# Optimization experiments

Hardware: AMD Instinct MI355X
Metric: run time of the kernel (lower is better)

Reference implementation:

```python
import jax, jax.numpy as jnp
import numpy as np

TEMPERATURE = 0.5
EPS = 1e-12  # matches torch F.normalize default eps


def _l2_normalize(x):
    norm = jnp.sqrt(jnp.sum(x * x, axis=1, keepdims=True))
    return x / jnp.maximum(norm, EPS)


def setup_inputs() -> dict:
    key = jax.random.key(0)
    k1, k2 = jax.random.split(key)
    proj_1 = jax.random.normal(k1, (4096, 128), dtype=jnp.float32)
    proj_2 = jax.random.normal(k2, (4096, 128), dtype=jnp.float32)
    return {"proj_1": proj_1, "proj_2": proj_2}


def reference(proj_1, proj_2):
    batch_size = proj_1.shape[0]
    z_i = _l2_normalize(proj_1)
    z_j = _l2_normalize(proj_2)
    reps = jnp.concatenate([z_i, z_j], axis=0)  # [2B, D], rows unit-norm
    # cosine similarity of unit-norm rows == dot product -> single matmul
    sim = reps @ reps.T  # [2B, 2B]
    # positives: diag offset +B and -B
    pos_ij = jnp.diagonal(sim, offset=batch_size)   # [B]
    pos_ji = jnp.diagonal(sim, offset=-batch_size)  # [B]
    positives = jnp.concatenate([pos_ij, pos_ji], axis=0)  # [2B]
    nominator = jnp.exp(positives / TEMPERATURE)
    n = 2 * batch_size
    mask = 1.0 - jnp.eye(n, dtype=sim.dtype)
    denominator = jnp.sum(mask * jnp.exp(sim / TEMPERATURE), axis=1)  # [2B]
    all_losses = -jnp.log(nominator / denominator)
    return jnp.sum(all_losses) / n
```

## Files before the change

kernel.cpp:

```cpp
#include <hip/hip_runtime.h>
#include <stdint.h>


#define TEMP 0.5f
#define EXP2_SCALE 2.885390081777927f

typedef __bf16 bf16_t;
typedef bf16_t bf16x8 __attribute__((ext_vector_type(8)));
typedef float floatx4 __attribute__((ext_vector_type(4)));

typedef __attribute__((address_space(3))) uint32_t lds_u32;
typedef const __attribute__((address_space(1))) uint32_t glb_u32;

__device__ __forceinline__ unsigned short f32_to_bf16(float f) {
    union { float f; uint32_t u; } v; v.f = f;
    uint32_t u = v.u;
    uint32_t r = (u + 0x7FFFu + ((u >> 16) & 1u)) >> 16;
    return (unsigned short)r;
}

__device__ __forceinline__ bf16x8 as_bf16x8(uint4 v) {
    union { uint4 u; bf16x8 b; } c; c.u = v; return c.b;
}

__global__ __launch_bounds__(256) void norm_pos_kernel(
        const float* __restrict__ p1, const float* __restrict__ p2,
        unsigned short* __restrict__ reps, float* __restrict__ pos,
        float* __restrict__ rowsum, int B) {
    if (threadIdx.x < 16) {
        int z = blockIdx.x * 16 + threadIdx.x;
        if (z < 2 * B) rowsum[z] = 0.f;
    }

    const int wave = threadIdx.x >> 6;
    const int lane = threadIdx.x & 63;
    const int half = lane >> 5;
    const int h    = lane & 31;
    const int i = blockIdx.x * 8 + wave * 2 + half;
    if (i >= B) return;

    float4 a = ((const float4*)(p1 + (size_t)i * 128))[h];
    float4 b = ((const float4*)(p2 + (size_t)i * 128))[h];
    float ss1 = a.x * a.x + a.y * a.y + a.z * a.z + a.w * a.w;
    float ss2 = b.x * b.x + b.y * b.y + b.z * b.z + b.w * b.w;
    float d   = a.x * b.x + a.y * b.y + a.z * b.z + a.w * b.w;
    #pragma unroll
    for (int off = 16; off > 0; off >>= 1) {
        ss1 += __shfl_xor(ss1, off);
        ss2 += __shfl_xor(ss2, off);
        d   += __shfl_xor(d,   off);
    }
    float rn1 = rsqrtf(fmaxf(ss1, 1e-24f));
    float rn2 = rsqrtf(fmaxf(ss2, 1e-24f));

    ((ushort4*)reps)[(size_t)i * 32 + h] = make_ushort4(
        f32_to_bf16(a.x * rn1), f32_to_bf16(a.y * rn1),
        f32_to_bf16(a.z * rn1), f32_to_bf16(a.w * rn1));
    ((ushort4*)reps)[(size_t)(B + i) * 32 + h] = make_ushort4(
        f32_to_bf16(b.x * rn2), f32_to_bf16(b.y * rn2),
        f32_to_bf16(b.z * rn2), f32_to_bf16(b.w * rn2));

    if (h == 0) pos[i] = d * rn1 * rn2;
}

__global__ __launch_bounds__(256) void simexp_kernel(
        const unsigned short* __restrict__ reps,
        float* __restrict__ rowsum, int nt) {
    const int tid  = threadIdx.x;
    const int wave = tid >> 6;
    const int lane = tid & 63;
    const int quad = lane >> 4;
    const int l16  = lane & 15;

    int rem = (int)blockIdx.x;
    int by = 0;
    while (rem >= nt - by) { rem -= nt - by; ++by; }
    const int bx = by + rem;
    const bool diag = (bx == by);

    const int rowWave = by * 128 + wave * 32;
    const int colBase = bx * 128;

    const uint4* g = (const uint4*)reps;

    __shared__ __align__(16) unsigned short bbuf[8][2048];
    __shared__ float lds_cs[4][128];

    lds_cs[wave][lane]      = 0.f;
    lds_cs[wave][lane + 64] = 0.f;

    const int s_ks  = tid >> 6;
    const int s_fl  = tid & 63;
    const int s_fq  = s_fl >> 4;
    const int s_f16 = s_fl & 15;
    #pragma unroll
    for (int ct = 0; ct < 8; ++ct) {
        const unsigned short* src = reps
            + (size_t)(colBase + ct * 16 + s_f16) * 128 + s_ks * 32 + s_fq * 8;
        __builtin_amdgcn_global_load_lds(
            (glb_u32*)src, (lds_u32*)&bbuf[ct][tid * 8], 16, 0, 0);
    }

    bf16x8 a[2][4];
    #pragma unroll
    for (int t = 0; t < 2; ++t)
        #pragma unroll
        for (int ks = 0; ks < 4; ++ks)
            a[t][ks] = as_bf16x8(g[(size_t)(rowWave + t * 16 + l16) * 16 + ks * 4 + quad]);

    float rs[2][4];
    #pragma unroll
    for (int t = 0; t < 2; ++t)
        #pragma unroll
        for (int r = 0; r < 4; ++r) rs[t][r] = 0.f;

    __syncthreads();

    #pragma unroll 2
    for (int ct = 0; ct < 8; ++ct) {
        bf16x8 b[4];
        #pragma unroll
        for (int ks = 0; ks < 4; ++ks)
            b[ks] = *(const bf16x8*)&bbuf[ct][ks * 512 + lane * 8];

        floatx4 acc[2];
        #pragma unroll
        for (int t = 0; t < 2; ++t) acc[t] = (floatx4){0.f, 0.f, 0.f, 0.f};
        #pragma unroll
        for (int ks = 0; ks < 4; ++ks)
            #pragma unroll
            for (int t = 0; t < 2; ++t)
                acc[t] = __builtin_amdgcn_mfma_f32_16x16x32_bf16(a[t][ks], b[ks], acc[t], 0, 0, 0);

        const int c = colBase + ct * 16 + l16;
        if (!diag) {
            float cs = 0.f;
            #pragma unroll
            for (int t = 0; t < 2; ++t)
                #pragma unroll
                for (int r = 0; r < 4; ++r) {
                    float e = exp2f(acc[t][r] * EXP2_SCALE);
                    rs[t][r] += e;
                    cs += e;
                }
            cs += __shfl_xor(cs, 16);
            cs += __shfl_xor(cs, 32);
            if (lane < 16) lds_cs[wave][ct * 16 + lane] += cs;
        } else {
            #pragma unroll
            for (int t = 0; t < 2; ++t) {
                const int rb = rowWave + t * 16 + quad * 4;
                #pragma unroll
                for (int r = 0; r < 4; ++r) {
                    float e = (rb + r == c) ? 0.f : exp2f(acc[t][r] * EXP2_SCALE);
                    rs[t][r] += e;
                }
            }
        }
    }

    #pragma unroll
    for (int off = 1; off < 16; off <<= 1)
        #pragma unroll
        for (int t = 0; t < 2; ++t)
            #pragma unroll
            for (int r = 0; r < 4; ++r)
                rs[t][r] += __shfl_xor(rs[t][r], off);

    if (l16 == 0) {
        #pragma unroll
        for (int t = 0; t < 2; ++t)
            #pragma unroll
            for (int r = 0; r < 4; ++r)
                atomicAdd(&rowsum[rowWave + t * 16 + quad * 4 + r], rs[t][r]);
    }

    if (!diag) {
        __syncthreads();
        if (tid < 128)
            atomicAdd(&rowsum[colBase + tid],
                      lds_cs[0][tid] + lds_cs[1][tid] + lds_cs[2][tid] + lds_cs[3][tid]);
    }
}

__global__ __launch_bounds__(1024) void finalize_kernel(
        const float* __restrict__ rowsum, const float* __restrict__ pos,
        float* __restrict__ out, int N2, int B) {
    float v = 0.f;
    const float4* r4 = (const float4*)rowsum;
    const int n4 = N2 >> 2;
    for (int k = threadIdx.x; k < n4; k += 1024) {
        float4 x = r4[k];
        v += logf(x.x) + logf(x.y) + logf(x.z) + logf(x.w);
    }
    float p = 0.f;
    const float4* p4 = (const float4*)pos;
    const int b4 = B >> 2;
    for (int i = threadIdx.x; i < b4; i += 1024) {
        float4 x = p4[i];
        p += x.x + x.y + x.z + x.w;
    }
    float local = v * (1.0f / (float)N2) - p * (1.0f / ((float)B * TEMP));

    #pragma unroll
    for (int off = 32; off > 0; off >>= 1) local += __shfl_xor(local, off);

    __shared__ float wsum[16];
    int wave = threadIdx.x >> 6, lane = threadIdx.x & 63;
    if (lane == 0) wsum[wave] = local;
    __syncthreads();
    if (threadIdx.x == 0) {
        float s = 0.f;
        for (int i = 0; i < 16; ++i) s += wsum[i];
        out[0] = s;
    }
}

extern "C" void kernel_launch(void* const* d_in, const int* in_sizes, int n_in,
                              void* d_out, int out_size, void* d_ws, size_t ws_size,
                              hipStream_t stream) {
    const float* p1 = (const float*)d_in[0];
    const float* p2 = (const float*)d_in[1];
    float* out = (float*)d_out;

    const int B  = in_sizes[0] / 128;
    const int N2 = 2 * B;

    unsigned short* reps = (unsigned short*)d_ws;
    float* rowsum = (float*)((char*)d_ws + (size_t)N2 * 256);
    float* pos    = rowsum + N2;

    norm_pos_kernel<<<dim3((B + 7) / 8), dim3(256), 0, stream>>>(p1, p2, reps, pos, rowsum, B);

    const int nt = N2 / 128;
    const int nb = nt * (nt + 1) / 2;
    simexp_kernel<<<dim3(nb), dim3(256), 0, stream>>>(reps, rowsum, nt);

    finalize_kernel<<<dim3(1), dim3(1024), 0, stream>>>(rowsum, pos, out, N2, B);
}
```

Before: 91.51 us.

## Fuse normalize, sim-exp and finalize into one cooperative persistent kernel

The three kernels are merged into one persistent kernel launched cooperatively. Grid-wide syncs separate the normalize, similarity-exp and log-reduce phases, and blocks loop over the triangular tile list. Column sums are now kept in registers and atomically added per lane instead of being staged in LDS. Raw v_exp/v_log intrinsics are used, and the final reduction is spread across blocks with an atomicAdd to the output. The aim is to remove launch gaps and the single-block finalize, at the cost of grid-sync overhead, more global atomics, and a three-launch fallback path.

Measured after the change: 205.1 us. 2.24x slower.

```diff
diff --git a/kernel.cpp b/kernel.cpp
--- a/kernel.cpp
+++ b/kernel.cpp
@@ -1,5 +1,8 @@
 #include <hip/hip_runtime.h>
+#include <hip/hip_cooperative_groups.h>
 #include <stdint.h>
+
+namespace cg = cooperative_groups;
 
 
 #define TEMP 0.5f
@@ -23,196 +26,189 @@
     union { uint4 u; bf16x8 b; } c; c.u = v; return c.b;
 }
 
-__global__ __launch_bounds__(256) void norm_pos_kernel(
+__device__ __forceinline__ float exp2_raw(float x) {
+#if __has_builtin(__builtin_amdgcn_exp2f)
+    return __builtin_amdgcn_exp2f(x);
+#else
+    float r; asm("v_exp_f32 %0, %1" : "=v"(r) : "v"(x)); return r;
+#endif
+}
+__device__ __forceinline__ float log2_raw(float x) {
+#if __has_builtin(__builtin_amdgcn_logf)
+    return __builtin_amdgcn_logf(x);
+#else
+    float r; asm("v_log_f32 %0, %1" : "=v"(r) : "v"(x)); return r;
+#endif
+}
+
+__global__ __launch_bounds__(256, 4) void fused_kernel(
         const float* __restrict__ p1, const float* __restrict__ p2,
-        unsigned short* __restrict__ reps, float* __restrict__ pos,
-        float* __restrict__ rowsum, int B) {
-    if (threadIdx.x < 16) {
-        int z = blockIdx.x * 16 + threadIdx.x;
-        if (z < 2 * B) rowsum[z] = 0.f;
-    }
-
-    const int wave = threadIdx.x >> 6;
-    const int lane = threadIdx.x & 63;
-    const int half = lane >> 5;
-    const int h    = lane & 31;
-    const int i = blockIdx.x * 8 + wave * 2 + half;
-    if (i >= B) return;
-
-    float4 a = ((const float4*)(p1 + (size_t)i * 128))[h];
-    float4 b = ((const float4*)(p2 + (size_t)i * 128))[h];
-    float ss1 = a.x * a.x + a.y * a.y + a.z * a.z + a.w * a.w;
-    float ss2 = b.x * b.x + b.y * b.y + b.z * b.z + b.w * b.w;
-    float d   = a.x * b.x + a.y * b.y + a.z * b.z + a.w * b.w;
-    #pragma unroll
-    for (int off = 16; off > 0; off >>= 1) {
-        ss1 += __shfl_xor(ss1, off);
-        ss2 += __shfl_xor(ss2, off);
-        d   += __shfl_xor(d,   off);
-    }
-    float rn1 = rsqrtf(fmaxf(ss1, 1e-24f));
-    float rn2 = rsqrtf(fmaxf(ss2, 1e-24f));
-
-    ((ushort4*)reps)[(size_t)i * 32 + h] = make_ushort4(
-        f32_to_bf16(a.x * rn1), f32_to_bf16(a.y * rn1),
-        f32_to_bf16(a.z * rn1), f32_to_bf16(a.w * rn1));
-    ((ushort4*)reps)[(size_t)(B + i) * 32 + h] = make_ushort4(
-        f32_to_bf16(b.x * rn2), f32_to_bf16(b.y * rn2),
-        f32_to_bf16(b.z * rn2), f32_to_bf16(b.w * rn2));
-
-    if (h == 0) pos[i] = d * rn1 * rn2;
-}
-
-__global__ __launch_bounds__(256) void simexp_kernel(
-        const unsigned short* __restrict__ reps,
-        float* __restrict__ rowsum, int nt) {
+        float* __restrict__ out, unsigned short* __restrict__ reps,
+        float* __restrict__ rowsum, float* __restrict__ pos,
+        int B, int nt, int nb, int phase) {
     const int tid  = threadIdx.x;
     const int wave = tid >> 6;
     const int lane = tid & 63;
     const int quad = lane >> 4;
     const int l16  = lane & 15;
-
-    int rem = (int)blockIdx.x;
-    int by = 0;
-    while (rem >= nt - by) { rem -= nt - by; ++by; }
-    const int bx = by + rem;
-    const bool diag = (bx == by);
-
-    const int rowWave = by * 128 + wave * 32;
-    const int colBase = bx * 128;
-
-    const uint4* g = (const uint4*)reps;
+    const int G    = gridDim.x;
+    const int N2   = 2 * B;
 
     __shared__ __align__(16) unsigned short bbuf[8][2048];
-    __shared__ float lds_cs[4][128];
-
-    lds_cs[wave][lane]      = 0.f;
-    lds_cs[wave][lane + 64] = 0.f;
-
-    const int s_ks  = tid >> 6;
-    const int s_fl  = tid & 63;
-    const int s_fq  = s_fl >> 4;
-    const int s_f16 = s_fl & 15;
-    #pragma unroll
-    for (int ct = 0; ct < 8; ++ct) {
-        const unsigned short* src = reps
-            + (size_t)(colBase + ct * 16 + s_f16) * 128 + s_ks * 32 + s_fq * 8;
-        __builtin_amdgcn_global_load_lds(
-            (glb_u32*)src, (lds_u32*)&bbuf[ct][tid * 8], 16, 0, 0);
-    }
-
-    bf16x8 a[2][4];
-    #pragma unroll
-    for (int t = 0; t < 2; ++t)
+    __shared__ float wsum[4];
+
+    if (phase <= 1) {
+        const int slot = tid >> 5;
+        const int h    = tid & 31;
+        for (int i = blockIdx.x * 8 + slot; i < B; i += G * 8) {
+            float4 a = ((const float4*)(p1 + (size_t)i * 128))[h];
+            float4 b = ((const float4*)(p2 + (size_t)i * 128))[h];
+            float ss1 = a.x*a.x + a.y*a.y + a.z*a.z + a.w*a.w;
+            float ss2 = b.x*b.x + b.y*b.y + b.z*b.z + b.w*b.w;
+            float d   = a.x*b.x + a.y*b.y + a.z*b.z + a.w*b.w;
+            #pragma unroll
+            for (int off = 16; off > 0; off >>= 1) {
+                ss1 += __shfl_xor(ss1, off);
+                ss2 += __shfl_xor(ss2, off);
+                d   += __shfl_xor(d,   off);
+            }
+            float rn1 = rsqrtf(fmaxf(ss1, 1e-24f));
+            float rn2 = rsqrtf(fmaxf(ss2, 1e-24f));
+            ((ushort4*)reps)[(size_t)i * 32 + h] = make_ushort4(
+                f32_to_bf16(a.x*rn1), f32_to_bf16(a.y*rn1),
+                f32_to_bf16(a.z*rn1), f32_to_bf16(a.w*rn1));
+            ((ushort4*)reps)[(size_t)(B + i) * 32 + h] = make_ushort4(
+                f32_to_bf16(b.x*rn2), f32_to_bf16(b.y*rn2),
+                f32_to_bf16(b.z*rn2), f32_to_bf16(b.w*rn2));
+            if (h == 0) pos[i] = d * rn1 * rn2;
+        }
+        for (int k = blockIdx.x * 256 + tid; k < N2; k += G * 256)
+            rowsum[k] = 0.f;
+        if (blockIdx.x == 0 && tid == 0) out[0] = 0.f;
+    }
+    if (phase == 0) cg::this_grid().sync();
+
+    if (phase == 0 || phase == 2) {
+        const uint4* g4 = (const uint4*)reps;
+        for (int t = blockIdx.x; t < nb; t += G) {
+            int rem = t, by = 0;
+            while (rem >= nt - by) { rem -= nt - by; ++by; }
+            const int bx = by + rem;
+            const bool diag = (bx == by);
+            const int rowWave = by * 128 + wave * 32;
+            const int colBase = bx * 128;
+
+            #pragma unroll
+            for (int ct = 0; ct < 8; ++ct) {
+                const unsigned short* src = reps
+                    + (size_t)(colBase + ct * 16 + l16) * 128 + wave * 32 + quad * 8;
+                __builtin_amdgcn_global_load_lds(
+                    (glb_u32*)src, (lds_u32*)&bbuf[ct][tid * 8], 16, 0, 0);
+            }
+
+            bf16x8 a[2][4];
+            #pragma unroll
+            for (int tt = 0; tt < 2; ++tt)
+                #pragma unroll
+                for (int ks = 0; ks < 4; ++ks)
+                    a[tt][ks] = as_bf16x8(
+                        g4[(size_t)(rowWave + tt * 16 + l16) * 16 + ks * 4 + quad]);
+
+            float rs[2][4];
+            #pragma unroll
+            for (int tt = 0; tt < 2; ++tt)
+                #pragma unroll
+                for (int r = 0; r < 4; ++r) rs[tt][r] = 0.f;
+            float csa[8];
+            #pragma unroll
+            for (int ct = 0; ct < 8; ++ct) csa[ct] = 0.f;
+
+            __syncthreads();
+
+            #pragma unroll
+            for (int ct = 0; ct < 8; ++ct) {
+                bf16x8 b[4];
+                #pragma unroll
+                for (int ks = 0; ks < 4; ++ks)
+                    b[ks] = *(const bf16x8*)&bbuf[ct][ks * 512 + lane * 8];
+
+                floatx4 acc[2];
+                acc[0] = (floatx4){0.f, 0.f, 0.f, 0.f};
+                acc[1] = (floatx4){0.f, 0.f, 0.f, 0.f};
+                #pragma unroll
+                for (int ks = 0; ks < 4; ++ks) {
+                    acc[0] = __builtin_amdgcn_mfma_f32_16x16x32_bf16(a[0][ks], b[ks], acc[0], 0, 0, 0);
+                    acc[1] = __builtin_amdgcn_mfma_f32_16x16x32_bf16(a[1][ks], b[ks], acc[1], 0, 0, 0);
+                }
+
+                if (!diag) {
+                    float cs = 0.f;
+                    #pragma unroll
+                    for (int tt = 0; tt < 2; ++tt)
+                        #pragma unroll
+                        for (int r = 0; r < 4; ++r) {
+                            float e = exp2_raw(acc[tt][r] * EXP2_SCALE);
+                            rs[tt][r] += e;
+                            cs += e;
+                        }
+                    cs += __shfl_xor(cs, 16);
+                    cs += __shfl_xor(cs, 32);
+                    csa[ct] = cs;
+                } else {
+                    const int c = colBase + ct * 16 + l16;
+                    #pragma unroll
+                    for (int tt = 0; tt < 2; ++tt) {
+                        const int rb = rowWave + tt * 16 + quad * 4;
+                        #pragma unroll
+                        for (int r = 0; r < 4; ++r) {
+                            float e = (rb + r == c) ? 0.f
+                                     : exp2_raw(acc[tt][r] * EXP2_SCALE);
+                            rs[tt][r] += e;
+                        }
+                    }
+                }
+            }
+
+            #pragma unroll
+            for (int off = 1; off < 16; off <<= 1)
+                #pragma unroll
+                for (int tt = 0; tt < 2; ++tt)
+                    #pragma unroll
+                    for (int r = 0; r < 4; ++r)
+                        rs[tt][r] += __shfl_xor(rs[tt][r], off);
+
+            if (l16 == 0) {
+                #pragma unroll
+                for (int tt = 0; tt < 2; ++tt)
+                    #pragma unroll
+                    for (int r = 0; r < 4; ++r)
+                        atomicAdd(&rowsum[rowWave + tt * 16 + quad * 4 + r], rs[tt][r]);
+            }
+            if (!diag && lane < 16) {
+                #pragma unroll
+                for (int ct = 0; ct < 8; ++ct)
+                    atomicAdd(&rowsum[colBase + ct * 16 + lane], csa[ct]);
+            }
+            __syncthreads();
+        }
+    }
+    if (phase == 0) cg::this_grid().sync();
+
+    if (phase == 0 || phase == 3) {
+        float vl = 0.f;
+        for (int k = blockIdx.x * 256 + tid; k < N2; k += G * 256)
+            vl += log2_raw(rowsum[k]);
+        float vp = 0.f;
+        for (int i = blockIdx.x * 256 + tid; i < B; i += G * 256)
+            vp += pos[i];
+        float local = vl * (0.6931471805599453f / (float)N2)
+                    - vp * (1.0f / ((float)B * TEMP));
         #pragma unroll
-        for (int ks = 0; ks < 4; ++ks)
-            a[t][ks] = as_bf16x8(g[(size_t)(rowWave + t * 16 + l16) * 16 + ks * 4 + quad]);
-
-    float rs[2][4];
-    #pragma unroll
-    for (int t = 0; t < 2; ++t)
-        #pragma unroll
-        for (int r = 0; r < 4; ++r) rs[t][r] = 0.f;
-
-    __syncthreads();
-
-    #pragma unroll 2
-    for (int ct = 0; ct < 8; ++ct) {
-        bf16x8 b[4];
-        #pragma unroll
-        for (int ks = 0; ks < 4; ++ks)
-            b[ks] = *(const bf16x8*)&bbuf[ct][ks * 512 + lane * 8];
-
-        floatx4 acc[2];
-        #pragma unroll
-        for (int t = 0; t < 2; ++t) acc[t] = (floatx4){0.f, 0.f, 0.f, 0.f};
-        #pragma unroll
-        for (int ks = 0; ks < 4; ++ks)
-            #pragma unroll
-            for (int t = 0; t < 2; ++t)
-                acc[t] = __builtin_amdgcn_mfma_f32_16x16x32_bf16(a[t][ks], b[ks], acc[t], 0, 0, 0);
-
-        const int c = colBase + ct * 16 + l16;
-        if (!diag) {
-            float cs = 0.f;
-            #pragma unroll
-            for (int t = 0; t < 2; ++t)
-                #pragma unroll
-                for (int r = 0; r < 4; ++r) {
-                    float e = exp2f(acc[t][r] * EXP2_SCALE);
-                    rs[t][r] += e;
-                    cs += e;
-                }
-            cs += __shfl_xor(cs, 16);
-            cs += __shfl_xor(cs, 32);
-            if (lane < 16) lds_cs[wave][ct * 16 + lane] += cs;
-        } else {
-            #pragma unroll
-            for (int t = 0; t < 2; ++t) {
-                const int rb = rowWave + t * 16 + quad * 4;
-                #pragma unroll
-                for (int r = 0; r < 4; ++r) {
-                    float e = (rb + r == c) ? 0.f : exp2f(acc[t][r] * EXP2_SCALE);
-                    rs[t][r] += e;
-                }
-            }
-        }
-    }
-
-    #pragma unroll
-    for (int off = 1; off < 16; off <<= 1)
-        #pragma unroll
-        for (int t = 0; t < 2; ++t)
-            #pragma unroll
-            for (int r = 0; r < 4; ++r)
-                rs[t][r] += __shfl_xor(rs[t][r], off);
-
-    if (l16 == 0) {
-        #pragma unroll
-        for (int t = 0; t < 2; ++t)
-            #pragma unroll
-            for (int r = 0; r < 4; ++r)
-                atomicAdd(&rowsum[rowWave + t * 16 + quad * 4 + r], rs[t][r]);
-    }
-
-    if (!diag) {
+        for (int off = 32; off > 0; off >>= 1) local += __shfl_xor(local, off);
+        if (lane == 0) wsum[wave] = local;
         __syncthreads();
-        if (tid < 128)
-            atomicAdd(&rowsum[colBase + tid],
-                      lds_cs[0][tid] + lds_cs[1][tid] + lds_cs[2][tid] + lds_cs[3][tid]);
-    }
-}
-
-__global__ __launch_bounds__(1024) void finalize_kernel(
-        const float* __restrict__ rowsum, const float* __restrict__ pos,
-        float* __restrict__ out, int N2, int B) {
-    float v = 0.f;
-    const float4* r4 = (const float4*)rowsum;
-    const int n4 = N2 >> 2;
-    for (int k = threadIdx.x; k < n4; k += 1024) {
-        float4 x = r4[k];
-        v += logf(x.x) + logf(x.y) + logf(x.z) + logf(x.w);
-    }
-    float p = 0.f;
-    const float4* p4 = (const float4*)pos;
-    const int b4 = B >> 2;
-    for (int i = threadIdx.x; i < b4; i += 1024) {
-        float4 x = p4[i];
-        p += x.x + x.y + x.z + x.w;
-    }
-    float local = v * (1.0f / (float)N2) - p * (1.0f / ((float)B * TEMP));
-
-    #pragma unroll
-    for (int off = 32; off > 0; off >>= 1) local += __shfl_xor(local, off);
-
-    __shared__ float wsum[16];
-    int wave = threadIdx.x >> 6, lane = threadIdx.x & 63;
-    if (lane == 0) wsum[wave] = local;
-    __syncthreads();
-    if (threadIdx.x == 0) {
-        float s = 0.f;
-        for (int i = 0; i < 16; ++i) s += wsum[i];
-        out[0] = s;
+        if (tid == 0)
+            atomicAdd(out, wsum[0] + wsum[1] + wsum[2] + wsum[3]);
     }
 }
 
@@ -230,11 +226,41 @@
     float* rowsum = (float*)((char*)d_ws + (size_t)N2 * 256);
     float* pos    = rowsum + N2;
 
-    norm_pos_kernel<<<dim3((B + 7) / 8), dim3(256), 0, stream>>>(p1, p2, reps, pos, rowsum, B);
-
     const int nt = N2 / 128;
     const int nb = nt * (nt + 1) / 2;
-    simexp_kernel<<<dim3(nb), dim3(256), 0, stream>>>(reps, rowsum, nt);
-
-    finalize_kernel<<<dim3(1), dim3(1024), 0, stream>>>(rowsum, pos, out, N2, B);
-}
+
+    static int gBlocks = 0;
+    if (gBlocks == 0) {
+        int dev = 0;
+        (void)hipGetDevice(&dev);
+        hipDeviceProp_t prop;
+        int ncu = 256;
+        if (hipGetDeviceProperties(&prop, dev) == hipSuccess &&
+            prop.multiProcessorCount > 0)
+            ncu = prop.multiProcessorCount;
+        int perCU = 0;
+        if (hipOccupancyMaxActiveBlocksPerMultiprocessor(
+                &perCU, reinterpret_cast<const void*>(fused_kernel), 256, 0)
+                != hipSuccess || perCU <= 0)
+            perCU = 2;
+        gBlocks = ncu * perCU;
+    }
+    int G = gBlocks;
+    if (G > nb) G = nb;
+
+    int Bv = B, ntv = nt, nbv = nb, phase0 = 0;
+    void* args[] = { (void*)&p1, (void*)&p2, (void*)&out, (void*)&reps,
+                     (void*)&rowsum, (void*)&pos, (void*)&Bv, (void*)&ntv,
+                     (void*)&nbv, (void*)&phase0 };
+    hipError_t err = hipLaunchCooperativeKernel(
+        reinterpret_cast<const void*>(fused_kernel),
+        dim3(G), dim3(256), args, 0, stream);
+    if (err != hipSuccess) {
+        fused_kernel<<<dim3((B + 7) / 8), dim3(256), 0, stream>>>(
+            p1, p2, out, reps, rowsum, pos, B, nt, nb, 1);
+        fused_kernel<<<dim3(nb), dim3(256), 0, stream>>>(
+            p1, p2, out, reps, rowsum, pos, B, nt, nb, 2);
+        fused_kernel<<<dim3(32), dim3(256), 0, stream>>>(
+            p1, p2, out, reps, rowsum, pos, B, nt, nb, 3);
+    }
+}
```
